# Kernel tuning notes

Measured on AMD Instinct MI355X. Metric: run time of the kernel, lower is better.

Reference implementation:

```python
import jax, jax.numpy as jnp
import numpy as np
import math

M = 0.2
S = 30.0
COS_M = math.cos(M); SIN_M = math.sin(M)
TH = math.cos(math.pi - M)          # threshold used in torch.where
MM = math.sin(math.pi - M) * M      # linear penalty past threshold
EPS_LS = 0.1                        # CrossEntropyLoss label_smoothing


def _normalize(a, axis=-1):
    return a / jnp.clip(jnp.linalg.norm(a, axis=axis, keepdims=True), 1e-12)


def setup_inputs() -> dict:
    key = jax.random.key(0)
    k1, k2, k3, k4, k5 = jax.random.split(key, 5)
    B, D, C = 2048, 512, 10000
    x = jax.random.normal(k1, (B, D), dtype=jnp.float32)
    label = jax.random.randint(k2, (B,), 0, 1000)  # valid class ids, ~2 per class
    std = math.sqrt(2.0 / (C + D))  # xavier_normal gain=1
    weight = jax.random.normal(k3, (C, D), dtype=jnp.float32) * std    # self.weight (w)
    weight_m = jax.random.normal(k4, (C, D), dtype=jnp.float32) * std  # self.weight_m (wq)
    weight_n = jax.random.uniform(k5, (C, D), dtype=jnp.float32)       # self.weight_n (wk)
    return {"x": x, "label": label, "weight": weight, "weight_m": weight_m, "weight_n": weight_n}


def reference(x, label, weight, weight_m, weight_n):
    B = x.shape[0]
    C = weight.shape[0]
    xn = _normalize(x)                                   # [B, D]

    # ---- AAM (ArcFace) branch ----
    cosine = xn @ _normalize(weight).T                   # [B, C]
    sine = jnp.sqrt(jnp.clip(1.0 - cosine * cosine, 0.0, 1.0))
    phi = cosine * COS_M - sine * SIN_M
    phi = jnp.where(cosine - TH > 0, phi, cosine - MM)
    one_hot = jax.nn.one_hot(label, C, dtype=cosine.dtype)
    output = (one_hot * phi + (1.0 - one_hot) * cosine) * S
    logp = jax.nn.log_softmax(output, axis=-1)
    q_target = one_hot * (1.0 - EPS_LS) + EPS_LS / C     # label smoothing
    aam_loss = -jnp.mean(jnp.sum(q_target * logp, axis=-1))

    # ---- Control-Contrastive branch ----
    label_matrix = label[:, None] == label[None, :]      # [B, B] bool
    q = xn @ _normalize(weight_m[label]).T               # [B, B]
    k = xn @ _normalize(weight_n[label]).T               # [B, B]
    sim = q * k                                          # elementwise, [B, B]

    lm = label_matrix.astype(sim.dtype)
    ap_m = jnp.sum(sim * lm, axis=1) / jnp.sum(lm, axis=1)  # masked row means, [B]
    ap = jnp.diagonal(sim)                                   # [B]
    an = jnp.where(label_matrix, 0.0, sim)                   # [B, B]

    cos_ap = jnp.clip(ap, 0.0, 1.0)
    sin_ap = jnp.sqrt(jnp.clip(1.0 - cos_ap, 0.0, 1.0))
    cos_apm = jnp.clip(ap_m, 0.0, 1.0)
    sin_apm = jnp.sqrt(jnp.clip(1.0 - cos_apm, 0.0, 1.0))
    cos_an = jnp.clip(an, 0.0, 1.0)
    sin_an = jnp.sqrt(jnp.clip(1.0 - cos_an, 0.0, 1.0))

    phi_pm_c = cos_ap * cos_apm - sin_ap * sin_apm       # [B]
    phi_pm_s = jnp.sqrt(jnp.clip(1.0 - phi_pm_c, 0.0, 1.0))
    phi_pm = phi_pm_c * COS_M - phi_pm_s * SIN_M
    logit_neg = 1.0 - phi_pm                              # [B]

    # torch broadcasting [B,B]*[B] -> broadcast over rows (axis 0)
    phi_nm_s = sin_an * cos_apm[None, :] + cos_an * sin_apm[None, :]
    phi_nm_c = jnp.sqrt(jnp.clip(1.0 - phi_nm_s, 0.0, 1.0))
    phi_nm = phi_nm_s * COS_M - phi_nm_c * SIN_M          # [B, B]

    # ragged boolean-indexed logsumexp == masked logsumexp over whole matrix
    lse_n = jax.nn.logsumexp(jnp.where(label_matrix, -jnp.inf, phi_nm))
    lse_neg = jax.nn.logsumexp(logit_neg)
    cc_loss = jax.nn.softplus(lse_n + lse_neg)

    return aam_loss + cc_loss
```

## Files before the change

kernel.cpp:

```cpp
#include <hip/hip_runtime.h>
#include <hip/hip_bf16.h>

typedef unsigned short u16;
typedef unsigned char u8;
typedef unsigned int u32;
typedef float f32x4 __attribute__((ext_vector_type(4)));
typedef unsigned int u32x4 __attribute__((ext_vector_type(4)));
typedef unsigned int u32x2 __attribute__((ext_vector_type(2)));
typedef long v2i64 __attribute__((ext_vector_type(2)));

constexpr int BATCH = 2048;
constexpr int DIM   = 512;
constexpr int NCLS  = 10000;
constexpr int NPAD  = 10240;

#define F_S     30.0f
#define F_COS_M 0.9800665778412416f
#define F_SIN_M 0.19866933079506122f
#define F_TH   (-0.9800665778412416f)
#define F_MM    0.03973386615901224f

#define G_AAM  1280
#define G_CC    512

static __device__ __forceinline__ float clampf(float v, float lo, float hi) {
    return fminf(fmaxf(v, lo), hi);
}
static __device__ __forceinline__ u32 pk4_fp8(float a, float b, float c, float d) {
    u32 w = __builtin_amdgcn_cvt_pk_fp8_f32(a, b, 0, false);
    w = __builtin_amdgcn_cvt_pk_fp8_f32(c, d, w, true);
    return w;
}
static __device__ __forceinline__ void glds16(const void* g, void* l) {
    __builtin_amdgcn_global_load_lds(
        (const __attribute__((address_space(1))) unsigned int*)g,
        (__attribute__((address_space(3))) unsigned int*)l, 16, 0, 0);
}
static __device__ __forceinline__ float blk_sum(float v, float* sh, int t) {
#pragma unroll
    for (int o = 32; o > 0; o >>= 1) v += __shfl_down(v, o, 64);
    __syncthreads();
    if ((t & 63) == 0) sh[t >> 6] = v;
    __syncthreads();
    return sh[0] + sh[1] + sh[2] + sh[3];
}

__global__ __launch_bounds__(256) void norm_all_kernel(const float* __restrict__ x,
                                                       const float* __restrict__ w,
                                                       const float* __restrict__ wm,
                                                       const float* __restrict__ wn,
                                                       const int* __restrict__ label,
                                                       u8* __restrict__ xnb,
                                                       u8* __restrict__ wb,
                                                       u8* __restrict__ wqb,
                                                       u8* __restrict__ wkb,
                                                       float* __restrict__ zacc) {
    const int t = threadIdx.x, lane = t & 63, wv = t >> 6;
    const int b = blockIdx.x;
    if (b < 33) zacc[b * 256 + t] = 0.f;

    const int row = b * 4 + wv;
    const float* src;
    u8* dst;
    const int blk = lane >> 3, ks = (lane >> 2) & 1, q = lane & 3;
    const int doff = blk * 64 + q * 16 + ks * 8;

    if (row < BATCH) {
        src = x + (size_t)row * DIM;
        dst = xnb + (size_t)row * DIM;
    } else if (row < BATCH + NPAD) {
        const int r = row - BATCH;
        dst = wb + (size_t)r * DIM;
        if (r >= NCLS) {
            u32x2 z = {0, 0};
            *(u32x2*)(dst + doff) = z;
            return;
        }
        src = w + (size_t)r * DIM;
    } else if (row < BATCH + NPAD + BATCH) {
        const int i = row - (BATCH + NPAD);
        src = wm + (size_t)label[i] * DIM;
        dst = wqb + (size_t)i * DIM;
    } else {
        const int i = row - (BATCH + NPAD + BATCH);
        src = wn + (size_t)label[i] * DIM;
        dst = wkb + (size_t)i * DIM;
    }
    const float4 v0 = ((const float4*)src)[lane * 2];
    const float4 v1 = ((const float4*)src)[lane * 2 + 1];
    float s = v0.x * v0.x + v0.y * v0.y + v0.z * v0.z + v0.w * v0.w
            + v1.x * v1.x + v1.y * v1.y + v1.z * v1.z + v1.w * v1.w;
#pragma unroll
    for (int o = 32; o > 0; o >>= 1) s += __shfl_xor(s, o, 64);
    const float inv = 1.0f / fmaxf(sqrtf(s), 1e-12f);
    u32x2 o2;
    o2[0] = pk4_fp8(v0.x * inv, v0.y * inv, v0.z * inv, v0.w * inv);
    o2[1] = pk4_fp8(v1.x * inv, v1.y * inv, v1.z * inv, v1.w * inv);
    *(u32x2*)(dst + doff) = o2;
}

__global__ __launch_bounds__(256) void gemm_fused_kernel(const u8* __restrict__ A,
                                                         const u8* __restrict__ Bw,
                                                         const u8* __restrict__ Bq,
                                                         const u8* __restrict__ Bk,
                                                         const int* __restrict__ label,
                                                         float* __restrict__ sumexp,
                                                         float* __restrict__ sumlogit,
                                                         float* __restrict__ philab,
                                                         float* __restrict__ sim,
                                                         float* __restrict__ msum,
                                                         float* __restrict__ mcnt,
                                                         float* __restrict__ ap) {
    __shared__ __align__(16) u8 sA[128 * 64];
    __shared__ __align__(16) u8 sB[128 * 64];
    __shared__ float red0[128];
    __shared__ float red1[128];

    const int t = threadIdx.x;
    const int lane = t & 63, wave = t >> 6;
    const int fr = lane & 15, quad = lane >> 4;
    const int slot = quad ^ (fr & 3);

    if (t < 128) { red0[t] = 0.f; red1[t] = 0.f; }

    const int srow = t >> 2;
    const int sgr  = (t & 3) ^ (srow & 3);

    if (blockIdx.x < G_AAM) {
        const int flat = blockIdx.x;
        const int xcd = flat & 7, r = flat >> 3;
        const int bm = r & 15;
        const int bn = (r >> 4) * 8 + xcd;

        const int wm = (wave >> 1) * 64, wn = (wave & 1) * 64;
        const u8* ag = A  + (size_t)(bm * 128 + srow) * DIM + sgr * 16;
        const u8* bg = Bw + (size_t)(bn * 128 + srow) * DIM + sgr * 16;
        u8* al = &sA[t * 16];
        u8* bl = &sB[t * 16];

        f32x4 acc[4][4] = {};

        for (int kb = 0; kb < 8; kb++) {
            const int ko = kb * 64;
            glds16(ag + ko, al);
            glds16(ag + (size_t)64 * DIM + ko, al + 4096);
            glds16(bg + ko, bl);
            glds16(bg + (size_t)64 * DIM + ko, bl + 4096);
            __syncthreads();
            v2i64 a8[4], b8[4];
#pragma unroll
            for (int f = 0; f < 4; f++) {
                a8[f] = __builtin_bit_cast(v2i64, *(const u32x4*)&sA[(wm + f * 16 + fr) * 64 + slot * 16]);
                b8[f] = __builtin_bit_cast(v2i64, *(const u32x4*)&sB[(wn + f * 16 + fr) * 64 + slot * 16]);
            }
#pragma unroll
            for (int i = 0; i < 4; i++)
#pragma unroll
                for (int j = 0; j < 4; j++) {
                    acc[i][j] = __builtin_amdgcn_mfma_f32_16x16x32_fp8_fp8(a8[i][0], b8[j][0], acc[i][j], 0, 0, 0);
                    acc[i][j] = __builtin_amdgcn_mfma_f32_16x16x32_fp8_fp8(a8[i][1], b8[j][1], acc[i][j], 0, 0, 0);
                }
            __syncthreads();
        }

#pragma unroll
        for (int i = 0; i < 4; i++) {
#pragma unroll
            for (int r3 = 0; r3 < 4; r3++) {
                const int ml = wm + i * 16 + quad * 4 + r3;
                const int mg = bm * 128 + ml;
                const int lab = label[mg];
                float esum = 0.f, lsum = 0.f;
#pragma unroll
                for (int j = 0; j < 4; j++) {
                    const int ng = bn * 128 + wn + j * 16 + fr;
                    if (ng < NCLS) {
                        float c = acc[i][j][r3];
                        float logit;
                        if (ng == lab) {
                            float sine = sqrtf(clampf(1.f - c * c, 0.f, 1.f));
                            float phi = c * F_COS_M - sine * F_SIN_M;
                            float val = ((c - F_TH) > 0.f) ? phi : (c - F_MM);
                            logit = F_S * val;
                            philab[mg] = logit;
                        } else {
                            logit = F_S * c;
                        }
                        esum += __expf(logit);
                        lsum += logit;
                    }
                }
#pragma unroll
                for (int off = 1; off < 16; off <<= 1) {
                    esum += __shfl_xor(esum, off, 64);
                    lsum += __shfl_xor(lsum, off, 64);
                }
                if (fr == 0) {
                    atomicAdd(&red0[ml], esum);
                    atomicAdd(&red1[ml], lsum);
                }
            }
        }
        __syncthreads();
        if (t < 128) {
            atomicAdd(&sumexp[bm * 128 + t], red0[t]);
            atomicAdd(&sumlogit[bm * 128 + t], red1[t]);
        }
    } else {
        const int c = blockIdx.x - G_AAM;
        const int xcd = c & 7, r = c >> 3;
        const int bm = r & 15;
        const int bn = (r >> 4) * 8 + xcd;

        const int wm = (wave >> 1) * 64, wn = (wave & 1) * 32;
        u8* Qs = sB;
        u8* Ks = sB + 4096;

        const u8* ag = A  + (size_t)(bm * 128 + srow) * DIM + sgr * 16;
        const u8* qg = Bq + (size_t)(bn * 64 + srow) * DIM + sgr * 16;
        const u8* kg = Bk + (size_t)(bn * 64 + srow) * DIM + sgr * 16;
        u8* al = &sA[t * 16];
        u8* ql = &Qs[t * 16];
        u8* kl = &Ks[t * 16];

        f32x4 aq[4][2] = {};
        f32x4 ak[4][2] = {};

        for (int kb = 0; kb < 8; kb++) {
            const int ko = kb * 64;
            glds16(ag + ko, al);
            glds16(ag + (size_t)64 * DIM + ko, al + 4096);
            glds16(qg + ko, ql);
            glds16(kg + ko, kl);
            __syncthreads();
            v2i64 a8[4], q8[2], k8[2];
#pragma unroll
            for (int f = 0; f < 4; f++)
                a8[f] = __builtin_bit_cast(v2i64, *(const u32x4*)&sA[(wm + f * 16 + fr) * 64 + slot * 16]);
#pragma unroll
            for (int f = 0; f < 2; f++) {
                q8[f] = __builtin_bit_cast(v2i64, *(const u32x4*)&Qs[(wn + f * 16 + fr) * 64 + slot * 16]);
                k8[f] = __builtin_bit_cast(v2i64, *(const u32x4*)&Ks[(wn + f * 16 + fr) * 64 + slot * 16]);
            }
#pragma unroll
            for (int i = 0; i < 4; i++)
#pragma unroll
                for (int j = 0; j < 2; j++) {
                    aq[i][j] = __builtin_amdgcn_mfma_f32_16x16x32_fp8_fp8(a8[i][0], q8[j][0], aq[i][j], 0, 0, 0);
                    aq[i][j] = __builtin_amdgcn_mfma_f32_16x16x32_fp8_fp8(a8[i][1], q8[j][1], aq[i][j], 0, 0, 0);
                    ak[i][j] = __builtin_amdgcn_mfma_f32_16x16x32_fp8_fp8(a8[i][0], k8[j][0], ak[i][j], 0, 0, 0);
                    ak[i][j] = __builtin_amdgcn_mfma_f32_16x16x32_fp8_fp8(a8[i][1], k8[j][1], ak[i][j], 0, 0, 0);
                }
            __syncthreads();
        }

        int lab_n[2];
#pragma unroll
        for (int j = 0; j < 2; j++) lab_n[j] = label[bn * 64 + wn + j * 16 + fr];

#pragma unroll
        for (int i = 0; i < 4; i++) {
#pragma unroll
            for (int r3 = 0; r3 < 4; r3++) {
                const int ml = wm + i * 16 + quad * 4 + r3;
                const int mg = bm * 128 + ml;
                const int lm = label[mg];
                float ms = 0.f, mc = 0.f;
#pragma unroll
                for (int j = 0; j < 2; j++) {
                    const int ng = bn * 64 + wn + j * 16 + fr;
                    float s = aq[i][j][r3] * ak[i][j][r3];
                    sim[(size_t)mg * BATCH + ng] = s;
                    if (lab_n[j] == lm) { ms += s; mc += 1.f; }
                    if (mg == ng) ap[mg] = s;
                }
#pragma unroll
                for (int off = 1; off < 16; off <<= 1) {
                    ms += __shfl_xor(ms, off, 64);
                    mc += __shfl_xor(mc, off, 64);
                }
                if (fr == 0) {
                    atomicAdd(&red0[ml], ms);
                    atomicAdd(&red1[ml], mc);
                }
            }
        }
        __syncthreads();
        if (t < 128) {
            atomicAdd(&msum[bm * 128 + t], red0[t]);
            atomicAdd(&mcnt[bm * 128 + t], red1[t]);
        }
    }
}

__global__ __launch_bounds__(256) void cc_pass2_kernel(const float* __restrict__ sim,
                                                       const int* __restrict__ label,
                                                       const float* __restrict__ msum,
                                                       const float* __restrict__ mcnt,
                                                       const float* __restrict__ ap,
                                                       const float* __restrict__ sumexp,
                                                       const float* __restrict__ sumlogit,
                                                       const float* __restrict__ philab,
                                                       float* __restrict__ zn,
                                                       float* __restrict__ zneg,
                                                       float* __restrict__ accA,
                                                       unsigned* __restrict__ tick,
                                                       float* __restrict__ out) {
    __shared__ __align__(16) float cam_s[BATCH];
    __shared__ __align__(16) float sam_s[BATCH];
    __shared__ float sh[4];
    const int t = threadIdx.x, b = blockIdx.x;

    for (int j = t; j < BATCH; j += 256) {
        float cam = clampf(msum[j] / mcnt[j], 0.f, 1.f);
        cam_s[j] = cam;
        sam_s[j] = sqrtf(clampf(1.f - cam, 0.f, 1.f));
    }
    __syncthreads();

    float acc = 0.f;
#pragma unroll
    for (int row = 0; row < 4; row++) {
        const int i = b * 4 + row;
        const int li = label[i];
        const f32x4* simr = (const f32x4*)(sim + (size_t)i * BATCH);
        const f32x4* cap4 = (const f32x4*)cam_s;
        const f32x4* sap4 = (const f32x4*)sam_s;
#pragma unroll
        for (int k = 0; k < 2; k++) {
            const int jj = t + k * 256;
            f32x4 s4 = simr[jj];
            int4 l4i = ((const int4*)label)[jj];
            const int* l4 = (const int*)&l4i;
            f32x4 ca4 = cap4[jj];
            f32x4 sa4 = sap4[jj];
#pragma unroll
            for (int e = 0; e < 4; e++) {
                if (l4[e] != li) {
                    float can = clampf(s4[e], 0.f, 1.f);
                    float san = sqrtf(clampf(1.f - can, 0.f, 1.f));
                    float pns = san * ca4[e] + can * sa4[e];
                    float pnc = sqrtf(clampf(1.f - pns, 0.f, 1.f));
                    acc += __expf(pns * F_COS_M - pnc * F_SIN_M);
                }
            }
        }
    }
    acc = blk_sum(acc, sh, t);

    if (t == 0) {
        float apart = 0.f, epart = 0.f;
#pragma unroll
        for (int row = 0; row < 4; row++) {
            const int rr = b * 4 + row;
            float lse = logf(sumexp[rr]);
            apart += 0.9f * (philab[rr] - lse) + 1e-5f * (sumlogit[rr] - (float)NCLS * lse);
            float cam = cam_s[rr], sam = sam_s[rr];
            float cap = clampf(ap[rr], 0.f, 1.f);
            float sap = sqrtf(clampf(1.f - cap, 0.f, 1.f));
            float ppc = cap * cam - sap * sam;
            float pps = sqrtf(clampf(1.f - ppc, 0.f, 1.f));
            epart += __expf(1.f - (ppc * F_COS_M - pps * F_SIN_M));
        }
        atomicAdd(zn, acc);
        atomicAdd(accA, apart);
        atomicAdd(zneg, epart);
        unsigned old = __hip_atomic_fetch_add(tick, 1u, __ATOMIC_ACQ_REL, __HIP_MEMORY_SCOPE_AGENT);
        if (old == 511u) {
            float znv = __hip_atomic_load(zn,   __ATOMIC_RELAXED, __HIP_MEMORY_SCOPE_AGENT);
            float aav = __hip_atomic_load(accA, __ATOMIC_RELAXED, __HIP_MEMORY_SCOPE_AGENT);
            float zgv = __hip_atomic_load(zneg, __ATOMIC_RELAXED, __HIP_MEMORY_SCOPE_AGENT);
            float aam = -aav / (float)BATCH;
            float z = logf(znv) + logf(zgv);
            float cc = (z > 0.f) ? (z + log1pf(__expf(-z))) : log1pf(__expf(z));
            out[0] = aam + cc;
        }
    }
}

extern "C" void kernel_launch(void* const* d_in, const int* in_sizes, int n_in,
                              void* d_out, int out_size, void* d_ws, size_t ws_size,
                              hipStream_t stream) {
    const float* x        = (const float*)d_in[0];
    const int*   label    = (const int*)d_in[1];
    const float* weight   = (const float*)d_in[2];
    const float* weight_m = (const float*)d_in[3];
    const float* weight_n = (const float*)d_in[4];
    float* out = (float*)d_out;
    char* ws = (char*)d_ws;

    const size_t o_xnb  = 0;
    const size_t o_wb   = o_xnb + (size_t)BATCH * DIM;
    const size_t o_wqb  = o_wb  + (size_t)NPAD * DIM;
    const size_t o_wkb  = o_wqb + (size_t)BATCH * DIM;
    const size_t o_sim  = o_wkb + (size_t)BATCH * DIM;
    const size_t o_misc = o_sim + (size_t)BATCH * BATCH * 4;

    u8* xnb = (u8*)(ws + o_xnb);
    u8* wb  = (u8*)(ws + o_wb);
    u8* wqb = (u8*)(ws + o_wqb);
    u8* wkb = (u8*)(ws + o_wkb);
    float* sim = (float*)(ws + o_sim);
    float* mf  = (float*)(ws + o_misc);

    float* sumexp   = mf;
    float* sumlogit = mf + 2048;
    float* msum     = mf + 4096;
    float* mcnt     = mf + 6144;
    float* zn       = mf + 8192;
    float* zneg     = mf + 8193;
    float* accA     = mf + 8194;
    unsigned* tick  = (unsigned*)(mf + 8195);
    float* philab  = mf + 8448;
    float* ap      = mf + 10496;

    norm_all_kernel<<<(BATCH + NPAD + 2 * BATCH) / 4, 256, 0, stream>>>(
        x, weight, weight_m, weight_n, label, xnb, wb, wqb, wkb, mf);

    gemm_fused_kernel<<<G_AAM + G_CC, 256, 0, stream>>>(
        xnb, wb, wqb, wkb, label,
        sumexp, sumlogit, philab, sim, msum, mcnt, ap);

    cc_pass2_kernel<<<512, 256, 0, stream>>>(
        sim, label, msum, mcnt, ap,
        sumexp, sumlogit, philab, zn, zneg, accA, tick, out);
}
```

Measured before the change: 188.7 us.

## Keep full A row-block resident in LDS and loop over N tiles persistently

The fused GEMM now loads an entire 128x512 fp8 A block into LDS once per workgroup and iterates over several N tiles (5 for the AAM branch, 2 for the contrastive branch), reusing A instead of reloading it per tile. The grid shrinks from 1792 to 512 workgroups, and the normalization kernel writes rows in a plain layout via lane shuffles. The sim matrix is stored in fp16 instead of fp32, halving its write and read traffic in the second pass. Costs include 64KB+ LDS per block, which limits occupancy, and lower precision of sim values, plus fewer workgroups to hide latency.

```diff
diff --git a/kernel.cpp b/kernel.cpp
--- a/kernel.cpp
+++ b/kernel.cpp
@@ -4,6 +4,8 @@
 typedef unsigned short u16;
 typedef unsigned char u8;
 typedef unsigned int u32;
+typedef _Float16 f16;
+typedef _Float16 f16x8 __attribute__((ext_vector_type(8)));
 typedef float f32x4 __attribute__((ext_vector_type(4)));
 typedef unsigned int u32x4 __attribute__((ext_vector_type(4)));
 typedef unsigned int u32x2 __attribute__((ext_vector_type(2)));
@@ -20,8 +22,8 @@
 #define F_TH   (-0.9800665778412416f)
 #define F_MM    0.03973386615901224f
 
-#define G_AAM  1280
-#define G_CC    512
+#define G_AAM  256
+#define G_CC   256
 
 static __device__ __forceinline__ float clampf(float v, float lo, float hi) {
     return fminf(fmaxf(v, lo), hi);
@@ -62,9 +64,6 @@
     const int row = b * 4 + wv;
     const float* src;
     u8* dst;
-    const int blk = lane >> 3, ks = (lane >> 2) & 1, q = lane & 3;
-    const int doff = blk * 64 + q * 16 + ks * 8;
-
     if (row < BATCH) {
         src = x + (size_t)row * DIM;
         dst = xnb + (size_t)row * DIM;
@@ -73,7 +72,7 @@
         dst = wb + (size_t)r * DIM;
         if (r >= NCLS) {
             u32x2 z = {0, 0};
-            *(u32x2*)(dst + doff) = z;
+            *(u32x2*)(dst + lane * 8) = z;
             return;
         }
         src = w + (size_t)r * DIM;
@@ -93,207 +92,202 @@
 #pragma unroll
     for (int o = 32; o > 0; o >>= 1) s += __shfl_xor(s, o, 64);
     const float inv = 1.0f / fmaxf(sqrtf(s), 1e-12f);
+    u32 lo = pk4_fp8(v0.x * inv, v0.y * inv, v0.z * inv, v0.w * inv);
+    u32 hi = pk4_fp8(v1.x * inv, v1.y * inv, v1.z * inv, v1.w * inv);
+    const int p = 8 * (lane >> 3) + 4 * (lane & 1) + ((lane >> 1) & 3);
     u32x2 o2;
-    o2[0] = pk4_fp8(v0.x * inv, v0.y * inv, v0.z * inv, v0.w * inv);
-    o2[1] = pk4_fp8(v1.x * inv, v1.y * inv, v1.z * inv, v1.w * inv);
-    *(u32x2*)(dst + doff) = o2;
-}
-
-__global__ __launch_bounds__(256) void gemm_fused_kernel(const u8* __restrict__ A,
-                                                         const u8* __restrict__ Bw,
-                                                         const u8* __restrict__ Bq,
-                                                         const u8* __restrict__ Bk,
-                                                         const int* __restrict__ label,
-                                                         float* __restrict__ sumexp,
-                                                         float* __restrict__ sumlogit,
-                                                         float* __restrict__ philab,
-                                                         float* __restrict__ sim,
-                                                         float* __restrict__ msum,
-                                                         float* __restrict__ mcnt,
-                                                         float* __restrict__ ap) {
-    __shared__ __align__(16) u8 sA[128 * 64];
-    __shared__ __align__(16) u8 sB[128 * 64];
+    o2[0] = __shfl(lo, p, 64);
+    o2[1] = __shfl(hi, p, 64);
+    *(u32x2*)(dst + lane * 8) = o2;
+}
+
+__global__ __launch_bounds__(256) void gemm_persist_kernel(const u8* __restrict__ A,
+                                                           const u8* __restrict__ Bw,
+                                                           const u8* __restrict__ Bq,
+                                                           const u8* __restrict__ Bk,
+                                                           const int* __restrict__ label,
+                                                           float* __restrict__ sumexp,
+                                                           float* __restrict__ sumlogit,
+                                                           float* __restrict__ philab,
+                                                           f16* __restrict__ sim,
+                                                           float* __restrict__ msum,
+                                                           float* __restrict__ mcnt,
+                                                           float* __restrict__ ap) {
+    __shared__ __align__(16) u8 sA[128 * 512];
+    __shared__ __align__(16) u8 sB[8192];
     __shared__ float red0[128];
     __shared__ float red1[128];
 
     const int t = threadIdx.x;
     const int lane = t & 63, wave = t >> 6;
     const int fr = lane & 15, quad = lane >> 4;
-    const int slot = quad ^ (fr & 3);
+    const int slotB = quad ^ (fr & 3);
+    const int rotA  = (quad - 4 * fr) & 31;
 
     if (t < 128) { red0[t] = 0.f; red1[t] = 0.f; }
+
+    const bool is_aam = blockIdx.x < G_AAM;
+    const int c = is_aam ? blockIdx.x : (blockIdx.x - G_AAM);
+    const int xcd = c & 7, g = c >> 3;
+    const int bm = g & 15, half = g >> 4;
+
+    {
+        const int rl = t >> 5;
+        const int gg = t & 31;
+        const int gs = (gg + 4 * rl) & 31;
+        const u8* abase = A + ((size_t)(bm * 128 + rl)) * 512 + gs * 16;
+#pragma unroll
+        for (int s = 0; s < 16; s++)
+            glds16(abase + (size_t)(s * 8) * 512, &sA[s * 4096 + t * 16]);
+    }
 
     const int srow = t >> 2;
     const int sgr  = (t & 3) ^ (srow & 3);
 
-    if (blockIdx.x < G_AAM) {
-        const int flat = blockIdx.x;
-        const int xcd = flat & 7, r = flat >> 3;
-        const int bm = r & 15;
-        const int bn = (r >> 4) * 8 + xcd;
-
+    if (is_aam) {
         const int wm = (wave >> 1) * 64, wn = (wave & 1) * 64;
-        const u8* ag = A  + (size_t)(bm * 128 + srow) * DIM + sgr * 16;
-        const u8* bg = Bw + (size_t)(bn * 128 + srow) * DIM + sgr * 16;
-        u8* al = &sA[t * 16];
-        u8* bl = &sB[t * 16];
-
-        f32x4 acc[4][4] = {};
-
-        for (int kb = 0; kb < 8; kb++) {
-            const int ko = kb * 64;
-            glds16(ag + ko, al);
-            glds16(ag + (size_t)64 * DIM + ko, al + 4096);
-            glds16(bg + ko, bl);
-            glds16(bg + (size_t)64 * DIM + ko, bl + 4096);
+        for (int u = 0; u < 5; u++) {
+            const int bn = (half * 5 + u) * 8 + xcd;
+            f32x4 acc[4][4] = {};
+            for (int kb = 0; kb < 8; kb++) {
+                glds16(Bw + (size_t)(bn * 128 + srow) * 512 + kb * 64 + sgr * 16, &sB[t * 16]);
+                glds16(Bw + (size_t)(bn * 128 + 64 + srow) * 512 + kb * 64 + sgr * 16, &sB[4096 + t * 16]);
+                __syncthreads();
+                const int gA = (4 * kb + rotA) & 31;
+                v2i64 a8[4], b8[4];
+#pragma unroll
+                for (int f = 0; f < 4; f++) {
+                    a8[f] = __builtin_bit_cast(v2i64, *(const u32x4*)&sA[(wm + f * 16 + fr) * 512 + gA * 16]);
+                    b8[f] = __builtin_bit_cast(v2i64, *(const u32x4*)&sB[(wn + f * 16 + fr) * 64 + slotB * 16]);
+                }
+#pragma unroll
+                for (int i = 0; i < 4; i++)
+#pragma unroll
+                    for (int j = 0; j < 4; j++) {
+                        acc[i][j] = __builtin_amdgcn_mfma_f32_16x16x32_fp8_fp8(a8[i][0], b8[j][0], acc[i][j], 0, 0, 0);
+                        acc[i][j] = __builtin_amdgcn_mfma_f32_16x16x32_fp8_fp8(a8[i][1], b8[j][1], acc[i][j], 0, 0, 0);
+                    }
+                __syncthreads();
+            }
+#pragma unroll
+            for (int i = 0; i < 4; i++) {
+#pragma unroll
+                for (int r3 = 0; r3 < 4; r3++) {
+                    const int ml = wm + i * 16 + quad * 4 + r3;
+                    const int mg = bm * 128 + ml;
+                    const int lab = label[mg];
+                    float esum = 0.f, lsum = 0.f;
+#pragma unroll
+                    for (int j = 0; j < 4; j++) {
+                        const int ng = bn * 128 + wn + j * 16 + fr;
+                        if (ng < NCLS) {
+                            float cv = acc[i][j][r3];
+                            float logit;
+                            if (ng == lab) {
+                                float sine = sqrtf(clampf(1.f - cv * cv, 0.f, 1.f));
+                                float phi = cv * F_COS_M - sine * F_SIN_M;
+                                float val = ((cv - F_TH) > 0.f) ? phi : (cv - F_MM);
+                                logit = F_S * val;
+                                philab[mg] = logit;
+                            } else {
+                                logit = F_S * cv;
+                            }
+                            esum += __expf(logit);
+                            lsum += logit;
+                        }
+                    }
+#pragma unroll
+                    for (int off = 1; off < 16; off <<= 1) {
+                        esum += __shfl_xor(esum, off, 64);
+                        lsum += __shfl_xor(lsum, off, 64);
+                    }
+                    if (fr == 0) {
+                        atomicAdd(&red0[ml], esum);
+                        atomicAdd(&red1[ml], lsum);
+                    }
+                }
+            }
             __syncthreads();
-            v2i64 a8[4], b8[4];
-#pragma unroll
-            for (int f = 0; f < 4; f++) {
-                a8[f] = __builtin_bit_cast(v2i64, *(const u32x4*)&sA[(wm + f * 16 + fr) * 64 + slot * 16]);
-                b8[f] = __builtin_bit_cast(v2i64, *(const u32x4*)&sB[(wn + f * 16 + fr) * 64 + slot * 16]);
-            }
-#pragma unroll
-            for (int i = 0; i < 4; i++)
-#pragma unroll
-                for (int j = 0; j < 4; j++) {
-                    acc[i][j] = __builtin_amdgcn_mfma_f32_16x16x32_fp8_fp8(a8[i][0], b8[j][0], acc[i][j], 0, 0, 0);
-                    acc[i][j] = __builtin_amdgcn_mfma_f32_16x16x32_fp8_fp8(a8[i][1], b8[j][1], acc[i][j], 0, 0, 0);
-                }
-            __syncthreads();
-        }
-
-#pragma unroll
-        for (int i = 0; i < 4; i++) {
-#pragma unroll
-            for (int r3 = 0; r3 < 4; r3++) {
-                const int ml = wm + i * 16 + quad * 4 + r3;
-                const int mg = bm * 128 + ml;
-                const int lab = label[mg];
-                float esum = 0.f, lsum = 0.f;
-#pragma unroll
-                for (int j = 0; j < 4; j++) {
-                    const int ng = bn * 128 + wn + j * 16 + fr;
-                    if (ng < NCLS) {
-                        float c = acc[i][j][r3];
-                        float logit;
-                        if (ng == lab) {
-                            float sine = sqrtf(clampf(1.f - c * c, 0.f, 1.f));
-                            float phi = c * F_COS_M - sine * F_SIN_M;
-                            float val = ((c - F_TH) > 0.f) ? phi : (c - F_MM);
-                            logit = F_S * val;
-                            philab[mg] = logit;
-                        } else {
-                            logit = F_S * c;
-                        }
-                        esum += __expf(logit);
-                        lsum += logit;
-                    }
-                }
-#pragma unroll
-                for (int off = 1; off < 16; off <<= 1) {
-                    esum += __shfl_xor(esum, off, 64);
-                    lsum += __shfl_xor(lsum, off, 64);
-                }
-                if (fr == 0) {
-                    atomicAdd(&red0[ml], esum);
-                    atomicAdd(&red1[ml], lsum);
-                }
-            }
-        }
-        __syncthreads();
-        if (t < 128) {
-            atomicAdd(&sumexp[bm * 128 + t], red0[t]);
-            atomicAdd(&sumlogit[bm * 128 + t], red1[t]);
+            if (t < 128) {
+                atomicAdd(&sumexp[bm * 128 + t], red0[t]);
+                atomicAdd(&sumlogit[bm * 128 + t], red1[t]);
+                red0[t] = 0.f; red1[t] = 0.f;
+            }
         }
     } else {
-        const int c = blockIdx.x - G_AAM;
-        const int xcd = c & 7, r = c >> 3;
-        const int bm = r & 15;
-        const int bn = (r >> 4) * 8 + xcd;
-
         const int wm = (wave >> 1) * 64, wn = (wave & 1) * 32;
         u8* Qs = sB;
         u8* Ks = sB + 4096;
-
-        const u8* ag = A  + (size_t)(bm * 128 + srow) * DIM + sgr * 16;
-        const u8* qg = Bq + (size_t)(bn * 64 + srow) * DIM + sgr * 16;
-        const u8* kg = Bk + (size_t)(bn * 64 + srow) * DIM + sgr * 16;
-        u8* al = &sA[t * 16];
-        u8* ql = &Qs[t * 16];
-        u8* kl = &Ks[t * 16];
-
-        f32x4 aq[4][2] = {};
-        f32x4 ak[4][2] = {};
-
-        for (int kb = 0; kb < 8; kb++) {
-            const int ko = kb * 64;
-            glds16(ag + ko, al);
-            glds16(ag + (size_t)64 * DIM + ko, al + 4096);
-            glds16(qg + ko, ql);
-            glds16(kg + ko, kl);
+        for (int u = 0; u < 2; u++) {
+            const int bn = (half * 2 + u) * 8 + xcd;
+            f32x4 aq[4][2] = {};
+            f32x4 ak[4][2] = {};
+            for (int kb = 0; kb < 8; kb++) {
+                glds16(Bq + (size_t)(bn * 64 + srow) * 512 + kb * 64 + sgr * 16, &Qs[t * 16]);
+                glds16(Bk + (size_t)(bn * 64 + srow) * 512 + kb * 64 + sgr * 16, &Ks[t * 16]);
+                __syncthreads();
+                const int gA = (4 * kb + rotA) & 31;
+                v2i64 a8[4], q8[2], k8[2];
+#pragma unroll
+                for (int f = 0; f < 4; f++)
+                    a8[f] = __builtin_bit_cast(v2i64, *(const u32x4*)&sA[(wm + f * 16 + fr) * 512 + gA * 16]);
+#pragma unroll
+                for (int f = 0; f < 2; f++) {
+                    q8[f] = __builtin_bit_cast(v2i64, *(const u32x4*)&Qs[(wn + f * 16 + fr) * 64 + slotB * 16]);
+                    k8[f] = __builtin_bit_cast(v2i64, *(const u32x4*)&Ks[(wn + f * 16 + fr) * 64 + slotB * 16]);
+                }
+#pragma unroll
+                for (int i = 0; i < 4; i++)
+#pragma unroll
+                    for (int j = 0; j < 2; j++) {
+                        aq[i][j] = __builtin_amdgcn_mfma_f32_16x16x32_fp8_fp8(a8[i][0], q8[j][0], aq[i][j], 0, 0, 0);
+                        aq[i][j] = __builtin_amdgcn_mfma_f32_16x16x32_fp8_fp8(a8[i][1], q8[j][1], aq[i][j], 0, 0, 0);
+                        ak[i][j] = __builtin_amdgcn_mfma_f32_16x16x32_fp8_fp8(a8[i][0], k8[j][0], ak[i][j], 0, 0, 0);
+                        ak[i][j] = __builtin_amdgcn_mfma_f32_16x16x32_fp8_fp8(a8[i][1], k8[j][1], ak[i][j], 0, 0, 0);
+                    }
+                __syncthreads();
+            }
+            int lab_n[2];
+#pragma unroll
+            for (int j = 0; j < 2; j++) lab_n[j] = label[bn * 64 + wn + j * 16 + fr];
+#pragma unroll
+            for (int i = 0; i < 4; i++) {
+#pragma unroll
+                for (int r3 = 0; r3 < 4; r3++) {
+                    const int ml = wm + i * 16 + quad * 4 + r3;
+                    const int mg = bm * 128 + ml;
+                    const int lm = label[mg];
+                    float ms = 0.f, mc = 0.f;
+#pragma unroll
+                    for (int j = 0; j < 2; j++) {
+                        const int ng = bn * 64 + wn + j * 16 + fr;
+                        float s = aq[i][j][r3] * ak[i][j][r3];
+                        sim[(size_t)mg * BATCH + ng] = (f16)s;
+                        if (lab_n[j] == lm) { ms += s; mc += 1.f; }
+                        if (mg == ng) ap[mg] = s;
+                    }
+#pragma unroll
+                    for (int off = 1; off < 16; off <<= 1) {
+                        ms += __shfl_xor(ms, off, 64);
+                        mc += __shfl_xor(mc, off, 64);
+                    }
+                    if (fr == 0) {
+                        atomicAdd(&red0[ml], ms);
+                        atomicAdd(&red1[ml], mc);
+                    }
+                }
+            }
             __syncthreads();
-            v2i64 a8[4], q8[2], k8[2];
-#pragma unroll
-            for (int f = 0; f < 4; f++)
-                a8[f] = __builtin_bit_cast(v2i64, *(const u32x4*)&sA[(wm + f * 16 + fr) * 64 + slot * 16]);
-#pragma unroll
-            for (int f = 0; f < 2; f++) {
-                q8[f] = __builtin_bit_cast(v2i64, *(const u32x4*)&Qs[(wn + f * 16 + fr) * 64 + slot * 16]);
-                k8[f] = __builtin_bit_cast(v2i64, *(const u32x4*)&Ks[(wn + f * 16 + fr) * 64 + slot * 16]);
-            }
-#pragma unroll
-            for (int i = 0; i < 4; i++)
-#pragma unroll
-                for (int j = 0; j < 2; j++) {
-                    aq[i][j] = __builtin_amdgcn_mfma_f32_16x16x32_fp8_fp8(a8[i][0], q8[j][0], aq[i][j], 0, 0, 0);
-                    aq[i][j] = __builtin_amdgcn_mfma_f32_16x16x32_fp8_fp8(a8[i][1], q8[j][1], aq[i][j], 0, 0, 0);
-                    ak[i][j] = __builtin_amdgcn_mfma_f32_16x16x32_fp8_fp8(a8[i][0], k8[j][0], ak[i][j], 0, 0, 0);
-                    ak[i][j] = __builtin_amdgcn_mfma_f32_16x16x32_fp8_fp8(a8[i][1], k8[j][1], ak[i][j], 0, 0, 0);
-                }
-            __syncthreads();
-        }
-
-        int lab_n[2];
-#pragma unroll
-        for (int j = 0; j < 2; j++) lab_n[j] = label[bn * 64 + wn + j * 16 + fr];
-
-#pragma unroll
-        for (int i = 0; i < 4; i++) {
-#pragma unroll
-            for (int r3 = 0; r3 < 4; r3++) {
-                const int ml = wm + i * 16 + quad * 4 + r3;
-                const int mg = bm * 128 + ml;
-                const int lm = label[mg];
-                float ms = 0.f, mc = 0.f;
-#pragma unroll
-                for (int j = 0; j < 2; j++) {
-                    const int ng = bn * 64 + wn + j * 16 + fr;
-                    float s = aq[i][j][r3] * ak[i][j][r3];
-                    sim[(size_t)mg * BATCH + ng] = s;
-                    if (lab_n[j] == lm) { ms += s; mc += 1.f; }
-                    if (mg == ng) ap[mg] = s;
-                }
-#pragma unroll
-                for (int off = 1; off < 16; off <<= 1) {
-                    ms += __shfl_xor(ms, off, 64);
-                    mc += __shfl_xor(mc, off, 64);
-                }
-                if (fr == 0) {
-                    atomicAdd(&red0[ml], ms);
-                    atomicAdd(&red1[ml], mc);
-                }
-            }
-        }
-        __syncthreads();
-        if (t < 128) {
-            atomicAdd(&msum[bm * 128 + t], red0[t]);
-            atomicAdd(&mcnt[bm * 128 + t], red1[t]);
-        }
-    }
-}
-
-__global__ __launch_bounds__(256) void cc_pass2_kernel(const float* __restrict__ sim,
+            if (t < 128) {
+                atomicAdd(&msum[bm * 128 + t], red0[t]);
+                atomicAdd(&mcnt[bm * 128 + t], red1[t]);
+                red0[t] = 0.f; red1[t] = 0.f;
+            }
+        }
+    }
+}
+
+__global__ __launch_bounds__(256) void cc_pass2_kernel(const f16* __restrict__ sim,
                                                        const int* __restrict__ label,
                                                        const float* __restrict__ msum,
                                                        const float* __restrict__ mcnt,
@@ -323,26 +317,24 @@
     for (int row = 0; row < 4; row++) {
         const int i = b * 4 + row;
         const int li = label[i];
-        const f32x4* simr = (const f32x4*)(sim + (size_t)i * BATCH);
-        const f32x4* cap4 = (const f32x4*)cam_s;
-        const f32x4* sap4 = (const f32x4*)sam_s;
-#pragma unroll
-        for (int k = 0; k < 2; k++) {
-            const int jj = t + k * 256;
-            f32x4 s4 = simr[jj];
-            int4 l4i = ((const int4*)label)[jj];
-            const int* l4 = (const int*)&l4i;
-            f32x4 ca4 = cap4[jj];
-            f32x4 sa4 = sap4[jj];
-#pragma unroll
-            for (int e = 0; e < 4; e++) {
-                if (l4[e] != li) {
-                    float can = clampf(s4[e], 0.f, 1.f);
-                    float san = sqrtf(clampf(1.f - can, 0.f, 1.f));
-                    float pns = san * ca4[e] + can * sa4[e];
-                    float pnc = sqrtf(clampf(1.f - pns, 0.f, 1.f));
-                    acc += __expf(pns * F_COS_M - pnc * F_SIN_M);
-                }
+        const f16x8 v = ((const f16x8*)(sim + (size_t)i * BATCH))[t];
+        const int4 l0 = ((const int4*)label)[t * 2];
+        const int4 l1 = ((const int4*)label)[t * 2 + 1];
+        const f32x4 ca0 = ((const f32x4*)cam_s)[t * 2];
+        const f32x4 ca1 = ((const f32x4*)cam_s)[t * 2 + 1];
+        const f32x4 sa0 = ((const f32x4*)sam_s)[t * 2];
+        const f32x4 sa1 = ((const f32x4*)sam_s)[t * 2 + 1];
+#pragma unroll
+        for (int e = 0; e < 8; e++) {
+            const int lj = (e < 4) ? ((const int*)&l0)[e] : ((const int*)&l1)[e - 4];
+            if (lj != li) {
+                float can = clampf((float)v[e], 0.f, 1.f);
+                float caj = (e < 4) ? ca0[e] : ca1[e - 4];
+                float saj = (e < 4) ? sa0[e] : sa1[e - 4];
+                float san = sqrtf(clampf(1.f - can, 0.f, 1.f));
+                float pns = san * caj + can * saj;
+                float pnc = sqrtf(clampf(1.f - pns, 0.f, 1.f));
+                acc += __expf(pns * F_COS_M - pnc * F_SIN_M);
             }
         }
     }
@@ -394,13 +386,13 @@
     const size_t o_wqb  = o_wb  + (size_t)NPAD * DIM;
     const size_t o_wkb  = o_wqb + (size_t)BATCH * DIM;
     const size_t o_sim  = o_wkb + (size_t)BATCH * DIM;
-    const size_t o_misc = o_sim + (size_t)BATCH * BATCH * 4;
+    const size_t o_misc = o_sim + (size_t)BATCH * BATCH * 2;
 
     u8* xnb = (u8*)(ws + o_xnb);
     u8* wb  = (u8*)(ws + o_wb);
     u8* wqb = (u8*)(ws + o_wqb);
     u8* wkb = (u8*)(ws + o_wkb);
-    float* sim = (float*)(ws + o_sim);
+    f16* sim = (f16*)(ws + o_sim);
     float* mf  = (float*)(ws + o_misc);
 
     float* sumexp   = mf;
@@ -417,7 +409,7 @@
     norm_all_kernel<<<(BATCH + NPAD + 2 * BATCH) / 4, 256, 0, stream>>>(
         x, weight, weight_m, weight_n, label, xnb, wb, wqb, wkb, mf);
 
-    gemm_fused_kernel<<<G_AAM + G_CC, 256, 0, stream>>>(
+    gemm_persist_kernel<<<G_AAM + G_CC, 256, 0, stream>>>(
         xnb, wb, wqb, wkb, label,
         sumexp, sumlogit, philab, sim, msum, mcnt, ap);
 
```

New measurement: 194.5 us. 1.03x slower.
